# Kernel optimization log

Hardware: AMD Instinct MI355X
Metric: run time of the kernel (lower is better)

The kernel has to match this reference:

```python
import jax, jax.numpy as jnp
import numpy as np

IN_DIM = 256
HIDDEN = 256
N_TAPES = 2
DIM = HIDDEN // N_TAPES          # 128
LSTM_H = 8 * N_TAPES             # 16
SEQ = 256
BATCH = 32
TAPELEN = 256


def setup_inputs() -> dict:
    key = jax.random.key(0)
    ks = jax.random.split(key, 10)
    s = 0.05
    inputs = jax.random.normal(ks[0], (SEQ, BATCH, IN_DIM), jnp.float32)
    # LSTM params (torch gate order: i, f, g, o)
    W_ih = s * jax.random.normal(ks[1], (4 * LSTM_H, IN_DIM), jnp.float32)
    W_hh = s * jax.random.normal(ks[2], (4 * LSTM_H, LSTM_H), jnp.float32)
    b_ih = s * jax.random.normal(ks[3], (4 * LSTM_H,), jnp.float32)
    b_hh = s * jax.random.normal(ks[4], (4 * LSTM_H,), jnp.float32)
    # value / out linear layers
    W_val = s * jax.random.normal(ks[5], (HIDDEN, IN_DIM), jnp.float32)
    b_val = s * jax.random.normal(ks[6], (HIDDEN,), jnp.float32)
    W_out = s * jax.random.normal(ks[7], (HIDDEN, HIDDEN), jnp.float32)
    b_out = s * jax.random.normal(ks[8], (HIDDEN,), jnp.float32)
    return {
        'inputs': inputs, 'tapelen': TAPELEN,
        'W_ih': W_ih, 'W_hh': W_hh, 'b_ih': b_ih, 'b_hh': b_hh,
        'W_val': W_val, 'b_val': b_val, 'W_out': W_out, 'b_out': b_out,
    }


def _lstm(inputs, W_ih, W_hh, b_ih, b_hh):
    # inputs: [S, B, in_dim] -> hidden seq [S, B, LSTM_H], torch gate order i,f,g,o
    S, B, _ = inputs.shape
    xg = inputs @ W_ih.T + (b_ih + b_hh)  # precompute input contribution [S,B,4H]

    def step(carry, xt):
        h, c = carry
        g = xt + h @ W_hh.T
        i, f, gg, o = jnp.split(g, 4, axis=-1)
        c = jax.nn.sigmoid(f) * c + jax.nn.sigmoid(i) * jnp.tanh(gg)
        h = jax.nn.sigmoid(o) * jnp.tanh(c)
        return (h, c), h

    h0 = jnp.zeros((B, W_hh.shape[1]), inputs.dtype)
    (_, _), hs = jax.lax.scan(step, (h0, h0), xg)
    return hs


def reference(inputs, tapelen, W_ih, W_hh, b_ih, b_hh, W_val, b_val, W_out, b_out):
    seqlen, bs, _ = inputs.shape
    values = (inputs @ W_val.T + b_val).reshape(seqlen, bs, N_TAPES, DIM)

    actions = _lstm(inputs, W_ih, W_hh, b_ih, b_hh).reshape(seqlen, bs, N_TAPES, 8)
    dirs_r = jax.nn.softmax(actions[..., 0:3], axis=-1)
    dirs_w = jax.nn.softmax(actions[..., 3:6], axis=-1)
    rwprobs = jax.nn.sigmoid(actions[..., 6:8])

    tape0 = jnp.zeros((tapelen, bs, N_TAPES, DIM), inputs.dtype)
    pos0 = jnp.zeros((tapelen, bs, N_TAPES), inputs.dtype).at[0].set(1.0)

    def step(carry, xs):
        tape, rpos, wpos = carry
        v, rd, wd, rw = xs  # v:[B,T,C] rd/wd:[B,T,3] rw:[B,T,2]
        # write: replace value at soft write position, gated by rw[...,1]
        oldval = jnp.einsum('lntc,lnt->ntc', tape, wpos)
        newmem = jnp.einsum('lnt,ntc->lntc', wpos, v - oldval)
        tape = tape + newmem * rw[None, :, :, 1:2]
        # NOTE: faithful to source — write-position shifts roll rpos, not wpos
        next_w = jnp.roll(rpos, 1, axis=0)
        prev_w = jnp.roll(rpos, -1, axis=0)
        wpos = prev_w * wd[None, :, :, 0] + wpos * wd[None, :, :, 1] + next_w * wd[None, :, :, 2]
        # read, gated by rw[...,0]
        read_out = jnp.einsum('lntc,lnt->ntc', tape, rpos * rw[None, :, :, 0])
        next_r = jnp.roll(rpos, 1, axis=0)
        prev_r = jnp.roll(rpos, -1, axis=0)
        rpos = prev_r * rd[None, :, :, 0] + rpos * rd[None, :, :, 1] + next_r * rd[None, :, :, 2]
        return (tape, rpos, wpos), read_out

    (tape, rpos, wpos), reads = jax.lax.scan(
        step, (tape0, pos0, pos0), (values, dirs_r, dirs_w, rwprobs))

    outputs = reads.reshape(seqlen, bs, HIDDEN) @ W_out.T + b_out
    return outputs, tape, (rpos, wpos)
```

## Files before the change

kernel.cpp:

```cpp
#include <hip/hip_runtime.h>

#define SEQ    256
#define BATCH  32
#define NT     2
#define DIM    128
#define LTAPE  256

typedef float f32x4 __attribute__((ext_vector_type(4)));
typedef short s16x8 __attribute__((ext_vector_type(8)));
typedef unsigned int u32;
typedef unsigned short u16;

__device__ __forceinline__ float sigm(float x) { return 1.f / (1.f + __expf(-x)); }
__device__ __forceinline__ float tanh_(float x) { float e = __expf(2.f * x); return 1.f - 2.f / (e + 1.f); }
__device__ __forceinline__ u16 f2bf(float x) {
  u32 u = __builtin_bit_cast(u32, x);
  u32 r = (u + 0x7fffu + ((u >> 16) & 1u)) >> 16;
  return (u16)r;
}
__device__ __forceinline__ float bf2f(u16 b) {
  u32 u = ((u32)b) << 16; return __builtin_bit_cast(float, u);
}

template<bool A_BF16, bool OUT_BF16>
__global__ __launch_bounds__(256) void gemm_mfma(
    const void* __restrict__ Av, const float* __restrict__ W,
    const float* __restrict__ bias, void* __restrict__ Cv, int N) {
  __shared__ u16 As[128 * 40];
  __shared__ u16 Bs[64 * 40];
  const int tid = threadIdx.x;
  const int bm = blockIdx.x * 128, bn = blockIdx.y * 64;
  const int wv = tid >> 6, lane = tid & 63;
  const int wm = wv >> 1, wn = wv & 1;
  const int l15 = lane & 15, l4 = lane >> 4;
  f32x4 acc[4][2] = {};
  const int arow = tid >> 1, ahalf = tid & 1;
  const int brow = (tid & 127) >> 1, bhalf = tid & 1;

  for (int k0 = 0; k0 < 256; k0 += 32) {
    u16 abuf[16];
    if (A_BF16) {
      const u16* A = (const u16*)Av;
      const uint4* p = (const uint4*)(A + (size_t)(bm + arow) * 256 + k0 + ahalf * 16);
      *(uint4*)(abuf) = p[0]; *(uint4*)(abuf + 8) = p[1];
    } else {
      const float* A = (const float*)Av;
      const float* src = A + (size_t)(bm + arow) * 256 + k0 + ahalf * 16;
      float4 x0 = ((const float4*)src)[0], x1 = ((const float4*)src)[1];
      float4 x2 = ((const float4*)src)[2], x3 = ((const float4*)src)[3];
      float xs[16] = {x0.x, x0.y, x0.z, x0.w, x1.x, x1.y, x1.z, x1.w,
                      x2.x, x2.y, x2.z, x2.w, x3.x, x3.y, x3.z, x3.w};
#pragma unroll
      for (int j = 0; j < 16; ++j) abuf[j] = f2bf(xs[j]);
    }
    u16 bbuf[16];
    if (tid < 128) {
      const float* src = W + (size_t)(bn + brow) * 256 + k0 + bhalf * 16;
      float4 x0 = ((const float4*)src)[0], x1 = ((const float4*)src)[1];
      float4 x2 = ((const float4*)src)[2], x3 = ((const float4*)src)[3];
      float xs[16] = {x0.x, x0.y, x0.z, x0.w, x1.x, x1.y, x1.z, x1.w,
                      x2.x, x2.y, x2.z, x2.w, x3.x, x3.y, x3.z, x3.w};
#pragma unroll
      for (int j = 0; j < 16; ++j) bbuf[j] = f2bf(xs[j]);
    }
    __syncthreads();
    *(uint4*)&As[arow * 40 + ahalf * 16] = *(const uint4*)(abuf);
    *(uint4*)&As[arow * 40 + ahalf * 16 + 8] = *(const uint4*)(abuf + 8);
    if (tid < 128) {
      *(uint4*)&Bs[brow * 40 + bhalf * 16] = *(const uint4*)(bbuf);
      *(uint4*)&Bs[brow * 40 + bhalf * 16 + 8] = *(const uint4*)(bbuf + 8);
    }
    __syncthreads();
    s16x8 af[4], bfr[2];
#pragma unroll
    for (int mi = 0; mi < 4; ++mi)
      af[mi] = *(const s16x8*)&As[(wm * 64 + mi * 16 + l15) * 40 + l4 * 8];
#pragma unroll
    for (int ni = 0; ni < 2; ++ni)
      bfr[ni] = *(const s16x8*)&Bs[(wn * 32 + ni * 16 + l15) * 40 + l4 * 8];
#pragma unroll
    for (int mi = 0; mi < 4; ++mi)
#pragma unroll
      for (int ni = 0; ni < 2; ++ni)
        acc[mi][ni] = __builtin_amdgcn_mfma_f32_16x16x32_bf16(af[mi], bfr[ni], acc[mi][ni], 0, 0, 0);
  }
#pragma unroll
  for (int mi = 0; mi < 4; ++mi)
#pragma unroll
    for (int ni = 0; ni < 2; ++ni)
#pragma unroll
      for (int r = 0; r < 4; ++r) {
        int row = bm + wm * 64 + mi * 16 + l4 * 4 + r;
        int col = bn + wn * 32 + ni * 16 + l15;
        float val = acc[mi][ni][r] + bias[col];
        if (OUT_BF16) ((u16*)Cv)[(size_t)row * N + col] = f2bf(val);
        else          ((float*)Cv)[(size_t)row * N + col] = val;
      }
}

template<bool PERM>
__global__ __launch_bounds__(256) void gemm_nt(
    const float* __restrict__ A, const float* __restrict__ W,
    const float* __restrict__ b1, const float* __restrict__ b2,
    float* __restrict__ C, int N) {
  __shared__ float Asm[16][68];
  __shared__ float Bsm[16][68];
  const int tid = threadIdx.x;
  const int bm = blockIdx.x * 64;
  const int bn = blockIdx.y * 64;
  const int lr = tid >> 2;
  const int lc4 = (tid & 3) * 4;
  const int tm = (tid & 15) * 4;
  const int tn = (tid >> 4) * 4;
  float acc[4][4];
#pragma unroll
  for (int i = 0; i < 4; ++i)
#pragma unroll
    for (int j = 0; j < 4; ++j) acc[i][j] = 0.f;
  int wr = bn + lr;
  if (PERM) wr = ((wr & 3) * 16) + (wr >> 2);
  for (int k0 = 0; k0 < 256; k0 += 16) {
    float4 av = *reinterpret_cast<const float4*>(&A[(bm + lr) * 256 + k0 + lc4]);
    float4 bv = *reinterpret_cast<const float4*>(&W[wr * 256 + k0 + lc4]);
    __syncthreads();
    Asm[lc4 + 0][lr] = av.x; Asm[lc4 + 1][lr] = av.y; Asm[lc4 + 2][lr] = av.z; Asm[lc4 + 3][lr] = av.w;
    Bsm[lc4 + 0][lr] = bv.x; Bsm[lc4 + 1][lr] = bv.y; Bsm[lc4 + 2][lr] = bv.z; Bsm[lc4 + 3][lr] = bv.w;
    __syncthreads();
#pragma unroll
    for (int kk = 0; kk < 16; ++kk) {
      float4 a = *reinterpret_cast<const float4*>(&Asm[kk][tm]);
      float4 b = *reinterpret_cast<const float4*>(&Bsm[kk][tn]);
      float a_[4] = {a.x, a.y, a.z, a.w};
      float b_[4] = {b.x, b.y, b.z, b.w};
#pragma unroll
      for (int i = 0; i < 4; ++i)
#pragma unroll
        for (int j = 0; j < 4; ++j) acc[i][j] += a_[i] * b_[j];
    }
  }
#pragma unroll
  for (int i = 0; i < 4; ++i)
#pragma unroll
    for (int j = 0; j < 4; ++j) {
      int n = bn + tn + j;
      int jm = PERM ? ((n & 3) * 16) + (n >> 2) : n;
      float bias = b1[jm] + (b2 ? b2[jm] : 0.f);
      C[(size_t)(bm + tm + i) * N + n] = acc[i][j] + bias;
    }
}

__global__ __launch_bounds__(64) void lstm_kernel(
    const float* __restrict__ xg,
    const float* __restrict__ W_hh,
    float* __restrict__ hout) {
  const int lane = threadIdx.x;
  const int b4 = lane >> 4, k = lane & 15;
  const int b = blockIdx.x * 4 + b4;
  const int lbase = lane & 48;
  float w[4][16];
#pragma unroll
  for (int q = 0; q < 4; ++q)
#pragma unroll
    for (int kk = 0; kk < 16; ++kk)
      w[q][kk] = W_hh[(q * 16 + k) * 16 + kk];
  float h = 0.f, c = 0.f;
  const float* xb = xg + (size_t)b * 64 + k * 4;
  float4 xA = *(const float4*)(xb + (size_t)0 * 2048);
  float4 xB = *(const float4*)(xb + (size_t)1 * 2048);
  float4 xC = *(const float4*)(xb + (size_t)2 * 2048);
  float4 xD = *(const float4*)(xb + (size_t)3 * 2048);

#define LSTM_STEP(S, XV)                                                     \
  {                                                                          \
    float hb[16];                                                            \
    _Pragma("unroll") for (int kk = 0; kk < 16; ++kk)                        \
      hb[kk] = __shfl(h, lbase + kk, 64);                                    \
    float g0 = XV.x, g1 = XV.y, g2 = XV.z, g3 = XV.w;                        \
    _Pragma("unroll") for (int kk = 0; kk < 16; ++kk) {                      \
      g0 += w[0][kk] * hb[kk];                                               \
      g1 += w[1][kk] * hb[kk];                                               \
      g2 += w[2][kk] * hb[kk];                                               \
      g3 += w[3][kk] * hb[kk];                                               \
    }                                                                        \
    c = sigm(g1) * c + sigm(g0) * tanh_(g2);                                 \
    h = sigm(g3) * tanh_(c);                                                 \
    hout[(size_t)((S) * 32 + b) * 16 + k] = h;                               \
  }

  for (int s0 = 0; s0 < SEQ; s0 += 4) {
    int p4 = s0 + 4; if (p4 > 255) p4 = 255;
    int p5 = s0 + 5; if (p5 > 255) p5 = 255;
    int p6 = s0 + 6; if (p6 > 255) p6 = 255;
    int p7 = s0 + 7; if (p7 > 255) p7 = 255;
    float4 nA = *(const float4*)(xb + (size_t)p4 * 2048);
    float4 nB = *(const float4*)(xb + (size_t)p5 * 2048);
    float4 nC = *(const float4*)(xb + (size_t)p6 * 2048);
    float4 nD = *(const float4*)(xb + (size_t)p7 * 2048);
    LSTM_STEP(s0 + 0, xA);
    LSTM_STEP(s0 + 1, xB);
    LSTM_STEP(s0 + 2, xC);
    LSTM_STEP(s0 + 3, xD);
    xA = nA; xB = nB; xC = nC; xD = nD;
  }
#undef LSTM_STEP
}

__global__ __launch_bounds__(256) void head_kernel(
    const float* __restrict__ hout,
    float* __restrict__ pc) {
  const int idx = blockIdx.x * 256 + threadIdx.x;
  const int e = idx & 7, s = (idx >> 3) & 255, p = idx >> 11;
  const int b = p >> 1, t = p & 1;
  const float* hp = hout + ((size_t)(s * 32 + b)) * 16 + t * 8;
  float outv;
  if (e < 3) {
    float a0 = hp[0], a1 = hp[1], a2 = hp[2];
    float m = fmaxf(a0, fmaxf(a1, a2));
    float e0 = __expf(a0 - m), e1 = __expf(a1 - m), e2 = __expf(a2 - m);
    float inv = 1.f / (e0 + e1 + e2);
    outv = (e == 0 ? e0 : (e == 1 ? e1 : e2)) * inv;
  } else if (e < 6) {
    float a3 = hp[3], a4 = hp[4], a5 = hp[5];
    float m = fmaxf(a3, fmaxf(a4, a5));
    float e0 = __expf(a3 - m), e1 = __expf(a4 - m), e2 = __expf(a5 - m);
    float inv = 1.f / (e0 + e1 + e2);
    outv = (e == 3 ? e0 : (e == 4 ? e1 : e2)) * inv;
  } else {
    outv = sigm(hp[e]);
  }
  pc[idx] = outv;
}

__global__ __launch_bounds__(64) void pos_kernel(
    const float* __restrict__ pc,
    float* __restrict__ posW, float* __restrict__ posRs,
    float* __restrict__ out_rpos, float* __restrict__ out_wpos) {
  const int p = blockIdx.x, lane = threadIdx.x;
  float r0 = 0, r1 = 0, r2 = 0, r3 = 0, w0 = 0, w1 = 0, w2 = 0, w3 = 0;
  if (lane == 0) { r0 = 1.f; w0 = 1.f; }
  const float* pcb = pc + (size_t)p * 2048;
  float4 c0 = *(const float4*)&pcb[0];
  float4 c1 = *(const float4*)&pcb[4];
  for (int s0 = 0; s0 < SEQ; s0 += 4) {
    float4 pf[8];
#pragma unroll
    for (int u = 0; u < 4; ++u) {
      int sn = s0 + u + 1; if (sn > 255) sn = 255;
      pf[2 * u]     = *(const float4*)&pcb[sn * 8];
      pf[2 * u + 1] = *(const float4*)&pcb[sn * 8 + 4];
    }
#pragma unroll
    for (int u = 0; u < 4; ++u) {
      const int s = s0 + u;
      size_t ob = ((size_t)p * 256 + s) * 256 + lane * 4;
      *(float4*)(posW + ob) = make_float4(w0, w1, w2, w3);
      float rw0 = c1.z;
      *(float4*)(posRs + ob) = make_float4(r0 * rw0, r1 * rw0, r2 * rw0, r3 * rw0);
      const float crd0 = c0.x, crd1 = c0.y, crd2 = c0.z;
      const float cwd0 = c0.w, cwd1 = c1.x, cwd2 = c1.y;
      float rn  = __shfl(r0, (lane + 1) & 63, 64);
      float rpv = __shfl(r3, (lane + 63) & 63, 64);
      float nw0 = r1 * cwd0 + w0 * cwd1 + rpv * cwd2;
      float nr0 = r1 * crd0 + r0 * crd1 + rpv * crd2;
      float nw1 = r2 * cwd0 + w1 * cwd1 + r0 * cwd2;
      float nr1 = r2 * crd0 + r1 * crd1 + r0 * crd2;
      float nw2 = r3 * cwd0 + w2 * cwd1 + r1 * cwd2;
      float nr2 = r3 * crd0 + r2 * crd1 + r1 * crd2;
      float nw3 = rn * cwd0 + w3 * cwd1 + r2 * cwd2;
      float nr3 = rn * crd0 + r3 * crd1 + r2 * crd2;
      r0 = nr0; r1 = nr1; r2 = nr2; r3 = nr3;
      w0 = nw0; w1 = nw1; w2 = nw2; w3 = nw3;
      c0 = pf[2 * u]; c1 = pf[2 * u + 1];
    }
  }
  out_rpos[(size_t)(lane * 4 + 0) * 64 + p] = r0;
  out_rpos[(size_t)(lane * 4 + 1) * 64 + p] = r1;
  out_rpos[(size_t)(lane * 4 + 2) * 64 + p] = r2;
  out_rpos[(size_t)(lane * 4 + 3) * 64 + p] = r3;
  out_wpos[(size_t)(lane * 4 + 0) * 64 + p] = w0;
  out_wpos[(size_t)(lane * 4 + 1) * 64 + p] = w1;
  out_wpos[(size_t)(lane * 4 + 2) * 64 + p] = w2;
  out_wpos[(size_t)(lane * 4 + 3) * 64 + p] = w3;
}

template<bool TRANS_A, bool B_NT, int MODE, int OUTK, int BROW>
__global__ __launch_bounds__(256) void bgemm(
    const float* __restrict__ A, const float* __restrict__ B,
    const float* __restrict__ pc, float* __restrict__ C,
    size_t sA, size_t sB) {
  __shared__ u16 Ah[128 * 40], Al[128 * 40], Bh[64 * 40], Bl[64 * 40];
  const int p = blockIdx.z;
  const int bm = blockIdx.y * 128, bn = blockIdx.x * 64;
  const int tid = threadIdx.x, wv = tid >> 6, lane = tid & 63;
  const int wm = wv >> 1, wn = wv & 1, l15 = lane & 15, l4 = lane >> 4;
  const int b = p >> 1, t = p & 1;

  if (MODE == 1 && bn >= bm + 128) return;
  if (MODE == 2 && bn >= bm + 128) {
#pragma unroll
    for (int mi = 0; mi < 4; ++mi)
#pragma unroll
      for (int ni = 0; ni < 2; ++ni)
#pragma unroll
        for (int r = 0; r < 4; ++r) {
          int row = bm + wm * 64 + mi * 16 + l4 * 4 + r;
          int col = bn + wn * 32 + ni * 16 + l15;
          C[(size_t)p * 65536 + (size_t)row * 256 + col] = 0.f;
        }
    return;
  }

  const float* Ap = A + (size_t)p * sA;
  const float* Bp = B + (size_t)p * sB;
  f32x4 acc[4][2] = {};

  for (int k0 = 0; k0 < 256; k0 += 32) {
    float xa[16];
    if (!TRANS_A) {
      const int m = tid >> 1, kq = (tid & 1) * 16;
      const float* src = Ap + (size_t)(bm + m) * 256 + k0 + kq;
#pragma unroll
      for (int j = 0; j < 4; ++j) *(float4*)(xa + j * 4) = ((const float4*)src)[j];
    } else {
      const int kr = tid >> 3, mq = (tid & 7) * 16;
      const float* src = Ap + (size_t)(k0 + kr) * 256 + bm + mq;
#pragma unroll
      for (int j = 0; j < 4; ++j) *(float4*)(xa + j * 4) = ((const float4*)src)[j];
    }
    u16 ah[16], al[16];
#pragma unroll
    for (int j = 0; j < 16; ++j) {
      u16 hh = f2bf(xa[j]);
      ah[j] = hh; al[j] = f2bf(xa[j] - bf2f(hh));
    }
    float xb[8];
    if (B_NT) {
      const int n = tid >> 2, kq = (tid & 3) * 8;
      const float* src = Bp + (size_t)(bn + n) * 256 + k0 + kq;
      *(float4*)(xb) = ((const float4*)src)[0];
      *(float4*)(xb + 4) = ((const float4*)src)[1];
    } else {
      const int kr = tid >> 3, nq = (tid & 7) * 8;
      const float* src = Bp + (size_t)(k0 + kr) * BROW + bn + nq;
      *(float4*)(xb) = ((const float4*)src)[0];
      *(float4*)(xb + 4) = ((const float4*)src)[1];
    }
    u16 bh[8], bl[8];
#pragma unroll
    for (int j = 0; j < 8; ++j) {
      u16 hh = f2bf(xb[j]);
      bh[j] = hh; bl[j] = f2bf(xb[j] - bf2f(hh));
    }
    __syncthreads();
    if (!TRANS_A) {
      const int m = tid >> 1, kq = (tid & 1) * 16;
      *(uint4*)&Ah[m * 40 + kq]     = *(const uint4*)(ah);
      *(uint4*)&Ah[m * 40 + kq + 8] = *(const uint4*)(ah + 8);
      *(uint4*)&Al[m * 40 + kq]     = *(const uint4*)(al);
      *(uint4*)&Al[m * 40 + kq + 8] = *(const uint4*)(al + 8);
    } else {
      const int kr = tid >> 3, mq = (tid & 7) * 16;
#pragma unroll
      for (int j = 0; j < 16; ++j) {
        Ah[(mq + j) * 40 + kr] = ah[j];
        Al[(mq + j) * 40 + kr] = al[j];
      }
    }
    if (B_NT) {
      const int n = tid >> 2, kq = (tid & 3) * 8;
      *(uint4*)&Bh[n * 40 + kq] = *(const uint4*)(bh);
      *(uint4*)&Bl[n * 40 + kq] = *(const uint4*)(bl);
    } else {
      const int kr = tid >> 3, nq = (tid & 7) * 8;
#pragma unroll
      for (int j = 0; j < 8; ++j) {
        Bh[(nq + j) * 40 + kr] = bh[j];
        Bl[(nq + j) * 40 + kr] = bl[j];
      }
    }
    __syncthreads();
    s16x8 fah[4], fal[4], fbh[2], fbl[2];
#pragma unroll
    for (int mi = 0; mi < 4; ++mi) {
      fah[mi] = *(const s16x8*)&Ah[(wm * 64 + mi * 16 + l15) * 40 + l4 * 8];
      fal[mi] = *(const s16x8*)&Al[(wm * 64 + mi * 16 + l15) * 40 + l4 * 8];
    }
#pragma unroll
    for (int ni = 0; ni < 2; ++ni) {
      fbh[ni] = *(const s16x8*)&Bh[(wn * 32 + ni * 16 + l15) * 40 + l4 * 8];
      fbl[ni] = *(const s16x8*)&Bl[(wn * 32 + ni * 16 + l15) * 40 + l4 * 8];
    }
#pragma unroll
    for (int mi = 0; mi < 4; ++mi)
#pragma unroll
      for (int ni = 0; ni < 2; ++ni) {
        acc[mi][ni] = __builtin_amdgcn_mfma_f32_16x16x32_bf16(fah[mi], fbh[ni], acc[mi][ni], 0, 0, 0);
        acc[mi][ni] = __builtin_amdgcn_mfma_f32_16x16x32_bf16(fah[mi], fbl[ni], acc[mi][ni], 0, 0, 0);
        acc[mi][ni] = __builtin_amdgcn_mfma_f32_16x16x32_bf16(fal[mi], fbh[ni], acc[mi][ni], 0, 0, 0);
      }
  }
#pragma unroll
  for (int mi = 0; mi < 4; ++mi)
#pragma unroll
    for (int ni = 0; ni < 2; ++ni)
#pragma unroll
      for (int r = 0; r < 4; ++r) {
        int row = bm + wm * 64 + mi * 16 + l4 * 4 + r;
        int col = bn + wn * 32 + ni * 16 + l15;
        float v = acc[mi][ni][r];
        if (MODE == 1) v = (col < row) ? v * pc[((size_t)p * 256 + row) * 8 + 7] : 0.f;
        if (MODE == 2) v = (col <= row) ? v : 0.f;
        if (OUTK == 0)      C[(size_t)p * 65536 + (size_t)row * 256 + col] = v;
        else if (OUTK == 1) C[((size_t)(row * 32 + b)) * 256 + t * 128 + col] = v;
        else                C[((size_t)row * 64 + p) * 128 + col] = v;
      }
}

__global__ __launch_bounds__(256) void solve_kernel(
    const float* __restrict__ L,
    const u16* __restrict__ values,
    const float* __restrict__ pc,
    float* __restrict__ delta) {
  const int p = blockIdx.x >> 1, half = blockIdx.x & 1;
  const int b = p >> 1, t = p & 1;
  const int tid = threadIdx.x, w = tid >> 6, lane = tid & 63;
  __shared__ float ds[256][64];
  __shared__ float Ps[32][64];
  __shared__ float Db[32][33];
  const float* Lp = L + (size_t)p * 65536;

  for (int k = 0; k < 8; ++k) {
    const int s0 = k * 32;
    float acc[8];
#pragma unroll
    for (int i = 0; i < 8; ++i) {
      const int s = s0 + w * 8 + i;
      float rv = bf2f(values[((size_t)(s * 32 + b)) * 256 + t * 128 + half * 64 + lane]);
      acc[i] = rv * pc[((size_t)p * 256 + s) * 8 + 7];
    }
    const float* Lr0 = Lp + (size_t)(s0 + w * 8) * 256;
#pragma unroll 4
    for (int j = 0; j < s0; ++j) {
      float dj = ds[j][lane];
#pragma unroll
      for (int i = 0; i < 8; ++i) acc[i] -= Lr0[(size_t)i * 256 + j] * dj;
    }
    {
      const int r = tid >> 3, q0 = (tid & 7) * 4;
      float4 dv = *(const float4*)(Lp + (size_t)(s0 + r) * 256 + s0 + q0);
      Db[r][q0] = dv.x; Db[r][q0 + 1] = dv.y; Db[r][q0 + 2] = dv.z; Db[r][q0 + 3] = dv.w;
    }
#pragma unroll
    for (int i = 0; i < 8; ++i) Ps[w * 8 + i][lane] = acc[i];
    __syncthreads();
    if (w == 0) {
      float d[32];
#pragma unroll
      for (int r = 0; r < 32; ++r) {
        float xa = Ps[r][lane], xb = 0.f;
#pragma unroll
        for (int q = 0; q < 32; ++q) {
          if (q < r) {
            if (q & 1) xb -= Db[r][q] * d[q];
            else       xa -= Db[r][q] * d[q];
          }
        }
        float x = xa + xb;
        d[r] = x;
        ds[s0 + r][lane] = x;
        delta[((size_t)p * 256 + s0 + r) * 128 + half * 64 + lane] = x;
      }
    }
    __syncthreads();
  }
}

extern "C" void kernel_launch(void* const* d_in, const int* in_sizes, int n_in,
                              void* d_out, int out_size, void* d_ws, size_t ws_size,
                              hipStream_t stream) {
  const float* inputs = (const float*)d_in[0];
  const float* W_ih = (const float*)d_in[2];
  const float* W_hh = (const float*)d_in[3];
  const float* b_ih = (const float*)d_in[4];
  const float* b_hh = (const float*)d_in[5];
  const float* W_val = (const float*)d_in[6];
  const float* b_val = (const float*)d_in[7];
  const float* W_out = (const float*)d_in[8];
  const float* b_out = (const float*)d_in[9];

  float* out = (float*)d_out;
  float* out_tape = out + 2097152;
  float* out_rpos = out + 4194304;
  float* out_wpos = out + 4210688;

  char* ws = (char*)d_ws;
  float* posW      = (float*)(ws);
  float* posRs     = (float*)(ws + 16777216);
  float* LHm       = (float*)(ws + 33554432);
  u16*   values_bf = (u16*)  (ws + 50331648);
  float* xg        = (float*)(ws + 54525952);
  float* delta     = (float*)(ws + 54525952);
  float* pcb       = (float*)(ws + 62914560);
  float* hout      = (float*)(ws + 63438848);
  float* reads_f32 = posRs;

  gemm_mfma<false, true><<<dim3(64, 4), 256, 0, stream>>>(inputs, W_val, b_val, values_bf, 256);
  gemm_nt<true><<<dim3(128, 1), 256, 0, stream>>>(inputs, W_ih, b_ih, b_hh, xg, 64);
  lstm_kernel<<<8, 64, 0, stream>>>(xg, W_hh, hout);
  head_kernel<<<512, 256, 0, stream>>>(hout, pcb);
  pos_kernel<<<64, 64, 0, stream>>>(pcb, posW, posRs, out_rpos, out_wpos);
  bgemm<false, true, 1, 0, 256><<<dim3(4, 2, 64), 256, 0, stream>>>(
      posW, posW, pcb, LHm, 65536, 65536);
  solve_kernel<<<128, 256, 0, stream>>>(LHm, values_bf, pcb, delta);
  bgemm<false, true, 2, 0, 256><<<dim3(4, 2, 64), 256, 0, stream>>>(
      posRs, posW, pcb, LHm, 65536, 65536);
  bgemm<false, false, 0, 1, 128><<<dim3(2, 2, 64), 256, 0, stream>>>(
      LHm, delta, pcb, reads_f32, 65536, 32768);
  bgemm<true, false, 0, 2, 128><<<dim3(2, 2, 64), 256, 0, stream>>>(
      posW, delta, pcb, out_tape, 65536, 32768);
  gemm_mfma<false, false><<<dim3(64, 4), 256, 0, stream>>>(reads_f32, W_out, b_out, out, 256);
}
```

Measured before the change: 453.5 us.

## Spread LSTM recurrence across one batch per wave with gate-per-lane layout

The LSTM recurrence kernel now runs one batch element per 64-lane wave (32 blocks instead of 8). Each lane computes one of the 64 gate pre-activations, and the results are exchanged with shuffles. The input-gate GEMM drops its column permutation to match the new natural gate layout. This shortens each serial step's dot-product chain and uses more CUs, at the cost of four extra shuffles per step and 48 lanes doing redundant nonlinearity work.

New measurement: 441.1 us. 1.03x faster.

```diff
diff --git a/kernel.cpp b/kernel.cpp
--- a/kernel.cpp
+++ b/kernel.cpp
@@ -98,7 +98,6 @@
       }
 }
 
-template<bool PERM>
 __global__ __launch_bounds__(256) void gemm_nt(
     const float* __restrict__ A, const float* __restrict__ W,
     const float* __restrict__ b1, const float* __restrict__ b2,
@@ -117,11 +116,9 @@
   for (int i = 0; i < 4; ++i)
 #pragma unroll
     for (int j = 0; j < 4; ++j) acc[i][j] = 0.f;
-  int wr = bn + lr;
-  if (PERM) wr = ((wr & 3) * 16) + (wr >> 2);
   for (int k0 = 0; k0 < 256; k0 += 16) {
     float4 av = *reinterpret_cast<const float4*>(&A[(bm + lr) * 256 + k0 + lc4]);
-    float4 bv = *reinterpret_cast<const float4*>(&W[wr * 256 + k0 + lc4]);
+    float4 bv = *reinterpret_cast<const float4*>(&W[(bn + lr) * 256 + k0 + lc4]);
     __syncthreads();
     Asm[lc4 + 0][lr] = av.x; Asm[lc4 + 1][lr] = av.y; Asm[lc4 + 2][lr] = av.z; Asm[lc4 + 3][lr] = av.w;
     Bsm[lc4 + 0][lr] = bv.x; Bsm[lc4 + 1][lr] = bv.y; Bsm[lc4 + 2][lr] = bv.z; Bsm[lc4 + 3][lr] = bv.w;
@@ -143,48 +140,49 @@
 #pragma unroll
     for (int j = 0; j < 4; ++j) {
       int n = bn + tn + j;
-      int jm = PERM ? ((n & 3) * 16) + (n >> 2) : n;
-      float bias = b1[jm] + (b2 ? b2[jm] : 0.f);
+      float bias = b1[n] + (b2 ? b2[n] : 0.f);
       C[(size_t)(bm + tm + i) * N + n] = acc[i][j] + bias;
     }
 }
 
-__global__ __launch_bounds__(64) void lstm_kernel(
+__global__ __launch_bounds__(64, 1) void lstm_kernel(
     const float* __restrict__ xg,
     const float* __restrict__ W_hh,
     float* __restrict__ hout) {
   const int lane = threadIdx.x;
-  const int b4 = lane >> 4, k = lane & 15;
-  const int b = blockIdx.x * 4 + b4;
-  const int lbase = lane & 48;
-  float w[4][16];
-#pragma unroll
-  for (int q = 0; q < 4; ++q)
-#pragma unroll
-    for (int kk = 0; kk < 16; ++kk)
-      w[q][kk] = W_hh[(q * 16 + k) * 16 + kk];
+  const int b = blockIdx.x;
+  const int k = lane & 15, q = lane >> 4;
+  float w[16];
+#pragma unroll
+  for (int kk = 0; kk < 16; ++kk) w[kk] = W_hh[lane * 16 + kk];
   float h = 0.f, c = 0.f;
-  const float* xb = xg + (size_t)b * 64 + k * 4;
-  float4 xA = *(const float4*)(xb + (size_t)0 * 2048);
-  float4 xB = *(const float4*)(xb + (size_t)1 * 2048);
-  float4 xC = *(const float4*)(xb + (size_t)2 * 2048);
-  float4 xD = *(const float4*)(xb + (size_t)3 * 2048);
+  const float* xb = xg + (size_t)b * 64 + lane;
+  float xA = xb[0 * 2048];
+  float xB = xb[1 * 2048];
+  float xC = xb[2 * 2048];
+  float xD = xb[3 * 2048];
 
 #define LSTM_STEP(S, XV)                                                     \
   {                                                                          \
     float hb[16];                                                            \
     _Pragma("unroll") for (int kk = 0; kk < 16; ++kk)                        \
-      hb[kk] = __shfl(h, lbase + kk, 64);                                    \
-    float g0 = XV.x, g1 = XV.y, g2 = XV.z, g3 = XV.w;                        \
-    _Pragma("unroll") for (int kk = 0; kk < 16; ++kk) {                      \
-      g0 += w[0][kk] * hb[kk];                                               \
-      g1 += w[1][kk] * hb[kk];                                               \
-      g2 += w[2][kk] * hb[kk];                                               \
-      g3 += w[3][kk] * hb[kk];                                               \
+      hb[kk] = __shfl(h, kk, 64);                                            \
+    float pa = w[0] * hb[0], pb = w[1] * hb[1];                              \
+    float pcc = w[2] * hb[2], pd = w[3] * hb[3];                             \
+    _Pragma("unroll") for (int kk = 4; kk < 16; kk += 4) {                   \
+      pa += w[kk + 0] * hb[kk + 0];                                         \
+      pb += w[kk + 1] * hb[kk + 1];                                         \
+      pcc += w[kk + 2] * hb[kk + 2];                                        \
+      pd += w[kk + 3] * hb[kk + 3];                                         \
     }                                                                        \
-    c = sigm(g1) * c + sigm(g0) * tanh_(g2);                                 \
-    h = sigm(g3) * tanh_(c);                                                 \
-    hout[(size_t)((S) * 32 + b) * 16 + k] = h;                               \
+    float g = XV + (pa + pb) + (pcc + pd);                                   \
+    float gi = __shfl(g, k, 64);                                             \
+    float gf = __shfl(g, 16 + k, 64);                                        \
+    float gg = __shfl(g, 32 + k, 64);                                        \
+    float go = __shfl(g, 48 + k, 64);                                        \
+    c = sigm(gf) * c + sigm(gi) * tanh_(gg);                                 \
+    h = sigm(go) * tanh_(c);                                                 \
+    if (q == 0) hout[(size_t)((S) * 32 + b) * 16 + k] = h;                   \
   }
 
   for (int s0 = 0; s0 < SEQ; s0 += 4) {
@@ -192,10 +190,10 @@
     int p5 = s0 + 5; if (p5 > 255) p5 = 255;
     int p6 = s0 + 6; if (p6 > 255) p6 = 255;
     int p7 = s0 + 7; if (p7 > 255) p7 = 255;
-    float4 nA = *(const float4*)(xb + (size_t)p4 * 2048);
-    float4 nB = *(const float4*)(xb + (size_t)p5 * 2048);
-    float4 nC = *(const float4*)(xb + (size_t)p6 * 2048);
-    float4 nD = *(const float4*)(xb + (size_t)p7 * 2048);
+    float nA = xb[(size_t)p4 * 2048];
+    float nB = xb[(size_t)p5 * 2048];
+    float nC = xb[(size_t)p6 * 2048];
+    float nD = xb[(size_t)p7 * 2048];
     LSTM_STEP(s0 + 0, xA);
     LSTM_STEP(s0 + 1, xB);
     LSTM_STEP(s0 + 2, xC);
@@ -231,7 +229,7 @@
   pc[idx] = outv;
 }
 
-__global__ __launch_bounds__(64) void pos_kernel(
+__global__ __launch_bounds__(64, 1) void pos_kernel(
     const float* __restrict__ pc,
     float* __restrict__ posW, float* __restrict__ posRs,
     float* __restrict__ out_rpos, float* __restrict__ out_wpos) {
@@ -505,8 +503,8 @@
   float* reads_f32 = posRs;
 
   gemm_mfma<false, true><<<dim3(64, 4), 256, 0, stream>>>(inputs, W_val, b_val, values_bf, 256);
-  gemm_nt<true><<<dim3(128, 1), 256, 0, stream>>>(inputs, W_ih, b_ih, b_hh, xg, 64);
-  lstm_kernel<<<8, 64, 0, stream>>>(xg, W_hh, hout);
+  gemm_nt<<<dim3(128, 1), 256, 0, stream>>>(inputs, W_ih, b_ih, b_hh, xg, 64);
+  lstm_kernel<<<32, 64, 0, stream>>>(xg, W_hh, hout);
   head_kernel<<<512, 256, 0, stream>>>(hout, pcb);
   pos_kernel<<<64, 64, 0, stream>>>(pcb, posW, posRs, out_rpos, out_wpos);
   bgemm<false, true, 1, 0, 256><<<dim3(4, 2, 64), 256, 0, stream>>>(
```
